# Performance work log

Measured on AMD Instinct MI355X. Metric: run time of the kernel, lower is better.

The kernel has to match this reference:

```python
import jax, jax.numpy as jnp
import numpy as np

B, C, H, W = 1, 256, 96, 96
C8 = C // 8
N = H * W


def setup_inputs() -> dict:
    key = jax.random.key(0)
    ks = jax.random.split(key, 12)
    inp = {
        "x": jax.random.normal(ks[0], (B, C, H, W), jnp.float32),
        "x_encoder": jax.random.normal(ks[1], (B, C, H, W), jnp.float32),
        # 1x1 conv params (weight stored as [out, in] matrices)
        "q_w": jax.random.normal(ks[2], (C8, C), jnp.float32) * 0.05,
        "q_b": jax.random.normal(ks[3], (C8,), jnp.float32) * 0.05,
        "k_w": jax.random.normal(ks[4], (C8, C), jnp.float32) * 0.05,
        "k_b": jax.random.normal(ks[5], (C8,), jnp.float32) * 0.05,
        "v_w": jax.random.normal(ks[6], (C, C), jnp.float32) * 0.05,
        "v_b": jax.random.normal(ks[7], (C,), jnp.float32) * 0.05,
        # positional bias parameters
        "h_pos": jax.random.normal(ks[8], (1, C8, H, 1), jnp.float32),
        "w_pos": jax.random.normal(ks[9], (1, C8, 1, W), jnp.float32),
        # gamma is zero-init in the module; use a random scalar for a non-trivial test
        "gamma": jax.random.normal(ks[10], (1,), jnp.float32),
    }
    return inp


def reference(x, x_encoder, q_w, q_b, k_w, k_b, v_w, v_b, h_pos, w_pos, gamma):
    b, c, h, w = x.shape
    n = h * w
    c8 = q_w.shape[0]
    # 1x1 convs == per-pixel linear maps
    query = (jnp.einsum('bchw,oc->bohw', x, q_w) + q_b[None, :, None, None])
    query = query.reshape(b, c8, n).transpose(0, 2, 1)            # [B, N, C8]
    key = (jnp.einsum('bchw,oc->bohw', x_encoder, k_w) + k_b[None, :, None, None])
    key = key.reshape(b, c8, n)                                   # [B, C8, N]
    # positional bias: broadcast-add then flatten, same as (height+width).view
    pos = (h_pos + w_pos).reshape(1, c8, n)                       # [1, C8, N]
    # energy = Q K^T + Q pos  ==  Q (K + pos)
    energy = jnp.einsum('bnc,bcm->bnm', query, key + pos)         # [B, N, N]
    attention = jax.nn.softmax(energy, axis=-1)
    value = (jnp.einsum('bchw,oc->bohw', x_encoder, v_w) + v_b[None, :, None, None])
    value = value.reshape(b, c, n)                                # [B, C, N]
    out = jnp.einsum('bcm,bnm->bcn', value, attention)            # [B, C, N]
    out = out.reshape(b, c, w, h)  # matches torch .view(B, C, W, H)
    return gamma * out + x
```

## Files before the change

### kernel.cpp

```cpp
#include <hip/hip_runtime.h>
#include <hip/hip_bf16.h>

#define NN 9216
#define CC 256
#define LOG2E 1.4426950408889634f

typedef __attribute__((ext_vector_type(8))) short short8;
typedef __attribute__((ext_vector_type(16))) float floatx16;
typedef __attribute__((ext_vector_type(4))) float floatx4;
typedef __attribute__((ext_vector_type(4))) unsigned short ushortx4;

#if __has_builtin(__builtin_amdgcn_exp2f)
#define fexp2 __builtin_amdgcn_exp2f
#else
#define fexp2 exp2f
#endif

__device__ __forceinline__ unsigned short f2bf(float f) {
    unsigned u = __float_as_uint(f);
    u = u + 0x7fffu + ((u >> 16) & 1u);
    return (unsigned short)(u >> 16);
}
__device__ __forceinline__ float bf2f(unsigned short s) {
    return __uint_as_float(((unsigned)s) << 16);
}
__device__ __forceinline__ unsigned pack2bf(float a, float b) {
    union { __hip_bfloat162 h; unsigned u; } cv;
    cv.h = __float22bfloat162_rn(make_float2(a, b));
    return cv.u;
}
__device__ __forceinline__ floatx16 mfma_bf16(short8 a, short8 b, floatx16 c) {
    return __builtin_amdgcn_mfma_f32_32x32x16_bf16(a, b, c, 0, 0, 0);
}

__global__ __launch_bounds__(256) void prep(
    const float* __restrict__ x, const float* __restrict__ xe,
    short* __restrict__ XBhi, short* __restrict__ XBlo,
    short* __restrict__ EBhi, short* __restrict__ EBlo)
{
    int t = threadIdx.x;
    const float* in = blockIdx.y ? xe : x;
    short* Dhi = blockIdx.y ? EBhi : XBhi;
    short* Dlo = blockIdx.y ? EBlo : XBlo;
    int tl = t & 31, sub = t >> 5;
    int nt = blockIdx.x >> 2, q4 = blockIdx.x & 3;
    int sub2 = q4 * 8 + sub;
    int kb_ = sub2 >> 1, hl = sub2 & 1;
    int n = nt * 32 + tl;
    int c0 = kb_ * 16 + hl * 8;
    union { unsigned short us[8]; short8 v8; } hi, lo;
#pragma unroll
    for (int j = 0; j < 8; ++j) {
        float val = in[(size_t)(c0 + j) * NN + n];
        unsigned short hb = f2bf(val);
        hi.us[j] = hb;
        lo.us[j] = f2bf(val - bf2f(hb));
    }
    size_t off = (((size_t)nt * 16 + kb_) * 64 + hl * 32 + tl) * 8;
    *(short8*)(Dhi + off) = hi.v8;
    *(short8*)(Dlo + off) = lo.v8;
}

__global__ __launch_bounds__(256) void wprep(
    const float* __restrict__ qw, const float* __restrict__ kw,
    const float* __restrict__ vw,
    short* __restrict__ WAhi, short* __restrict__ WAlo)
{
    int g = blockIdx.x * 256 + threadIdx.x;
    int lane = g & 63, kb_ = (g >> 6) & 15, ot = g >> 10;
    int o = lane & 31, half = lane >> 5;
    int c0 = kb_ * 16 + half * 8;
    const float* wsrc;
    int orow;
    float scale = 1.f;
    if (ot == 0) { wsrc = qw; orow = o; scale = LOG2E; }
    else if (ot == 1) { wsrc = kw; orow = o; }
    else { wsrc = vw; orow = (ot - 2) * 32 + o; }
    union { unsigned short us[8]; short8 v8; } hi, lo;
#pragma unroll
    for (int j = 0; j < 8; ++j) {
        float val = wsrc[(size_t)orow * 256 + c0 + j] * scale;
        unsigned short hb = f2bf(val);
        hi.us[j] = hb;
        lo.us[j] = f2bf(val - bf2f(hb));
    }
    size_t off = (((size_t)ot * 16 + kb_) * 64 + lane) * 8;
    *(short8*)(WAhi + off) = hi.v8;
    *(short8*)(WAlo + off) = lo.v8;
}

__global__ __launch_bounds__(256) void gemm_all(
    const short* __restrict__ XBhi, const short* __restrict__ XBlo,
    const short* __restrict__ EBhi, const short* __restrict__ EBlo,
    const short* __restrict__ WAhi, const short* __restrict__ WAlo,
    const float* __restrict__ qb, const float* __restrict__ kb,
    const float* __restrict__ hpos, const float* __restrict__ wpos,
    const float* __restrict__ vb,
    short* __restrict__ Qhi, short* __restrict__ Qlo,
    short* __restrict__ KP2, short* __restrict__ VF)
{
    __shared__ float lds[4][1024];
    int t = threadIdx.x;
    int wv = t >> 6, lane = t & 63, ln = lane & 31, h = lane >> 5;
    int nt = blockIdx.x * 2 + (wv & 1);
    int tile = blockIdx.y * 2 + (wv >> 1);

    const short* Bhi = (tile == 0 ? XBhi : EBhi) + (size_t)nt * 8192 + lane * 8;
    const short* Blo = (tile == 0 ? XBlo : EBlo) + (size_t)nt * 8192 + lane * 8;
    const short* Ahi = WAhi + (size_t)tile * 8192 + lane * 8;
    const short* Alo = WAlo + (size_t)tile * 8192 + lane * 8;

    floatx16 D;
#pragma unroll
    for (int r = 0; r < 16; ++r) D[r] = 0.f;
#pragma unroll
    for (int k = 0; k < 16; ++k) {
        short8 bh = *(const short8*)(Bhi + k * 512);
        short8 bl = *(const short8*)(Blo + k * 512);
        short8 ah = *(const short8*)(Ahi + k * 512);
        short8 al = *(const short8*)(Alo + k * 512);
        D = mfma_bf16(ah, bh, D);
        D = mfma_bf16(ah, bl, D);
        D = mfma_bf16(al, bh, D);
    }

    float* L = lds[wv];
#pragma unroll
    for (int r = 0; r < 16; ++r) {
        int row = (r & 3) + 8 * (r >> 2) + 4 * h;
        L[row * 32 + ((ln + row) & 31)] = D[r];
    }
    __syncthreads();

    if (tile == 0) {
        int n = nt * 32 + ln;
#pragma unroll
        for (int it = 0; it < 2; ++it) {
            int j0 = it * 16 + h * 8;
            union { unsigned short us[8]; short8 v8; } qh_, ql_;
#pragma unroll
            for (int jj = 0; jj < 8; ++jj) {
                int row = j0 + jj;
                float d = L[row * 32 + ((ln + row) & 31)] + qb[row] * LOG2E;
                unsigned short hb = f2bf(d);
                qh_.us[jj] = hb;
                ql_.us[jj] = f2bf(d - bf2f(hb));
            }
            *(short8*)(Qhi + (size_t)n * 32 + j0) = qh_.v8;
            *(short8*)(Qlo + (size_t)n * 32 + j0) = ql_.v8;
        }
    } else if (tile == 1) {
        int n = nt * 32 + ln;
        int hh = ((n >> 5) * 683) >> 11;
        int ww = n - hh * 96;
#pragma unroll
        for (int it = 0; it < 2; ++it) {
            int jb0 = it * 16 + h * 8;
            union { unsigned short us[8]; short8 v8; } o;
#pragma unroll
            for (int jj = 0; jj < 8; ++jj) {
                int row = jb0 + jj;
                float d = L[row * 32 + ((ln + row) & 31)]
                        + kb[row] + hpos[row * 96 + hh] + wpos[row * 96 + ww];
                o.us[jj] = f2bf(d);
            }
            *(short8*)(KP2 + (size_t)nt * 1024 + it * 512 + h * 256 + ln * 8) = o.v8;
        }
    } else {
        int cc = tile - 2;
        float bias = vb[cc * 32 + ln];
#pragma unroll
        for (int it = 0; it < 2; ++it) {
            union { unsigned short us[8]; short8 v8; } o;
#pragma unroll
            for (int ee = 0; ee < 8; ++ee) {
                int ml = it * 16 + h * 8 + ee;
                float d = L[ln * 32 + ((ml + ln) & 31)];
                o.us[ee] = f2bf(d + bias);
            }
            *(short8*)(VF + ((size_t)(nt * 2 + it) * 8 + cc) * 512 + lane * 8) = o.v8;
        }
    }
}

#define FSTEP(AH0, AH1, M0) do {                                                      \
    const size_t mo_ = (size_t)(M0) * 256;                                            \
    short8 va0 = *(const short8*)(Vb + mo_);                                          \
    short8 va1 = *(const short8*)(Vb + mo_ + 512);                                    \
    short8 va2 = *(const short8*)(Vb + mo_ + 1024);                                   \
    short8 va3 = *(const short8*)(Vb + mo_ + 1536);                                   \
    floatx16 S = {0.f,0.f,0.f,0.f,0.f,0.f,0.f,0.f,0.f,0.f,0.f,0.f,0.f,0.f,0.f,0.f};  \
    S = mfma_bf16(AH0, qf00, S);                                                      \
    S = mfma_bf16(AH0, qf01, S);                                                      \
    S = mfma_bf16(AH1, qf10, S);                                                      \
    S = mfma_bf16(AH1, qf11, S);                                                      \
    short8 va4 = *(const short8*)(Vb + mo_ + 2048);                                   \
    short8 va5 = *(const short8*)(Vb + mo_ + 2560);                                   \
    short8 va6 = *(const short8*)(Vb + mo_ + 3072);                                   \
    short8 va7 = *(const short8*)(Vb + mo_ + 3584);                                   \
    float ps = 0.f;                                                                   \
    _Pragma("unroll") for (int r = 0; r < 16; ++r) { S[r] = fexp2(S[r]); ps += S[r]; } \
    ps += __shfl_xor(ps, 32); l_run += ps;                                            \
    unsigned w0 = pack2bf(S[0], S[1]),  w1 = pack2bf(S[2], S[3]);                     \
    unsigned w2 = pack2bf(S[4], S[5]),  w3 = pack2bf(S[6], S[7]);                     \
    unsigned w4 = pack2bf(S[8], S[9]),  w5 = pack2bf(S[10], S[11]);                   \
    unsigned w6 = pack2bf(S[12], S[13]), w7 = pack2bf(S[14], S[15]);                  \
    {   unsigned p0 = h ? w0 : w2, p1 = h ? w1 : w3;                                  \
        unsigned e0 = (unsigned)__shfl_xor((int)p0, 32);                              \
        unsigned e1 = (unsigned)__shfl_xor((int)p1, 32);                              \
        union { unsigned u[4]; short8 v; } pf;                                        \
        pf.u[0] = h ? e0 : w0; pf.u[1] = h ? e1 : w1;                                 \
        pf.u[2] = h ? w2 : e0; pf.u[3] = h ? w3 : e1;                                 \
        O0 = mfma_bf16(va0, pf.v, O0); O1 = mfma_bf16(va1, pf.v, O1);                 \
        O2 = mfma_bf16(va2, pf.v, O2); O3 = mfma_bf16(va3, pf.v, O3);                 \
        O4 = mfma_bf16(va4, pf.v, O4); O5 = mfma_bf16(va5, pf.v, O5);                 \
        O6 = mfma_bf16(va6, pf.v, O6); O7 = mfma_bf16(va7, pf.v, O7); }               \
    short8 vb0 = *(const short8*)(Vb + mo_ + 4096);                                   \
    short8 vb1 = *(const short8*)(Vb + mo_ + 4608);                                   \
    short8 vb2 = *(const short8*)(Vb + mo_ + 5120);                                   \
    short8 vb3 = *(const short8*)(Vb + mo_ + 5632);                                   \
    short8 vb4 = *(const short8*)(Vb + mo_ + 6144);                                   \
    short8 vb5 = *(const short8*)(Vb + mo_ + 6656);                                   \
    short8 vb6 = *(const short8*)(Vb + mo_ + 7168);                                   \
    short8 vb7 = *(const short8*)(Vb + mo_ + 7680);                                   \
    {   unsigned p0 = h ? w4 : w6, p1 = h ? w5 : w7;                                  \
        unsigned e0 = (unsigned)__shfl_xor((int)p0, 32);                              \
        unsigned e1 = (unsigned)__shfl_xor((int)p1, 32);                              \
        union { unsigned u[4]; short8 v; } pf;                                        \
        pf.u[0] = h ? e0 : w4; pf.u[1] = h ? e1 : w5;                                 \
        pf.u[2] = h ? w6 : e0; pf.u[3] = h ? w7 : e1;                                 \
        O0 = mfma_bf16(vb0, pf.v, O0); O1 = mfma_bf16(vb1, pf.v, O1);                 \
        O2 = mfma_bf16(vb2, pf.v, O2); O3 = mfma_bf16(vb3, pf.v, O3);                 \
        O4 = mfma_bf16(vb4, pf.v, O4); O5 = mfma_bf16(vb5, pf.v, O5);                 \
        O6 = mfma_bf16(vb6, pf.v, O6); O7 = mfma_bf16(vb7, pf.v, O7); }               \
} while (0)

#define OW(G, OG) { _Pragma("unroll") for (int r = 0; r < 16; ++r) Osh[((G)*16 + r)*64 + lane] = OG[r]; }
#define OR(G, OG) { _Pragma("unroll") for (int r = 0; r < 16; ++r) OG[r] += Osh[((G)*16 + r)*64 + lane]; }
#define OGW(G, OG) { _Pragma("unroll") for (int r = 0; r < 16; ++r) { \
    int row = 32*(G) + (r & 3) + 8*(r >> 2) + 4*h;                    \
    Opart[obase + (size_t)row * NN + n0 + ln] = f2bf(OG[r]); } }

__global__ __launch_bounds__(256, 2) void flash(
    const short* __restrict__ Qhi, const short* __restrict__ Qlo,
    const short* __restrict__ KP2, const short* __restrict__ VT2,
    unsigned short* __restrict__ Opart,
    float* __restrict__ Mpart, float* __restrict__ Lpart)
{
    __shared__ float Osh[8192];
    __shared__ float Lsh[4][32];

    int t = threadIdx.x;
    int wv = t >> 6;
    int lane = t & 63;
    int ln = lane & 31;
    int h = lane >> 5;
    int nt = blockIdx.x >> 2, mq = blockIdx.x & 3;
    int n0 = nt * 32;
    int mw = mq * 2304 + wv * 576;

    int qoff = (n0 + ln) * 32 + h * 8;
    short8 qf00 = *(const short8*)(Qhi + qoff);
    short8 qf10 = *(const short8*)(Qhi + qoff + 16);
    short8 qf01 = *(const short8*)(Qlo + qoff);
    short8 qf11 = *(const short8*)(Qlo + qoff + 16);

    const short* Vb  = VT2 + (size_t)mw * 256 + (size_t)lane * 8;
    const short* KPb = KP2 + (size_t)mw * 32 + (size_t)lane * 8;

    floatx16 O0, O1, O2, O3, O4, O5, O6, O7;
#pragma unroll
    for (int r = 0; r < 16; ++r) {
        O0[r] = 0.f; O1[r] = 0.f; O2[r] = 0.f; O3[r] = 0.f;
        O4[r] = 0.f; O5[r] = 0.f; O6[r] = 0.f; O7[r] = 0.f;
    }
    float l_run = 0.f;

    short8 ahA0 = *(const short8*)(KPb);
    short8 ahA1 = *(const short8*)(KPb + 512);
    short8 ahB0, ahB1;

    for (int sp = 0; sp < 9; ++sp) {
        int m0 = sp * 64;
        ahB0 = *(const short8*)(KPb + (size_t)(m0 + 32) * 32);
        ahB1 = *(const short8*)(KPb + (size_t)(m0 + 32) * 32 + 512);
        FSTEP(ahA0, ahA1, m0);
        int nm = (sp < 8) ? (m0 + 64) : 0;
        ahA0 = *(const short8*)(KPb + (size_t)nm * 32);
        ahA1 = *(const short8*)(KPb + (size_t)nm * 32 + 512);
        FSTEP(ahB0, ahB1, m0 + 32);
    }

    if (lane < 32) Lsh[wv][ln] = l_run;
    __syncthreads();
    if (wv == 1) { OW(0,O0) OW(1,O1) OW(2,O2) OW(3,O3) OW(4,O4) OW(5,O5) OW(6,O6) OW(7,O7) }
    __syncthreads();
    if (wv == 0) { OR(0,O0) OR(1,O1) OR(2,O2) OR(3,O3) OR(4,O4) OR(5,O5) OR(6,O6) OR(7,O7) }
    __syncthreads();
    if (wv == 2) { OW(0,O0) OW(1,O1) OW(2,O2) OW(3,O3) OW(4,O4) OW(5,O5) OW(6,O6) OW(7,O7) }
    __syncthreads();
    if (wv == 0) { OR(0,O0) OR(1,O1) OR(2,O2) OR(3,O3) OR(4,O4) OR(5,O5) OR(6,O6) OR(7,O7) }
    __syncthreads();
    if (wv == 3) { OW(0,O0) OW(1,O1) OW(2,O2) OW(3,O3) OW(4,O4) OW(5,O5) OW(6,O6) OW(7,O7) }
    __syncthreads();
    if (wv == 0) {
        OR(0,O0) OR(1,O1) OR(2,O2) OR(3,O3) OR(4,O4) OR(5,O5) OR(6,O6) OR(7,O7)
        if (lane < 32) {
            Mpart[mq * NN + n0 + ln] = 0.f;
            Lpart[mq * NN + n0 + ln] = Lsh[0][ln] + Lsh[1][ln] + Lsh[2][ln] + Lsh[3][ln];
        }
        size_t obase = (size_t)mq * ((size_t)CC * NN);
        OGW(0,O0) OGW(1,O1) OGW(2,O2) OGW(3,O3) OGW(4,O4) OGW(5,O5) OGW(6,O6) OGW(7,O7)
    }
}

__global__ __launch_bounds__(256) void stats(
    const float* __restrict__ Mpart, const float* __restrict__ Lpart,
    const float* __restrict__ gamma, float* __restrict__ W)
{
    int n = blockIdx.x * 256 + threadIdx.x;
    float m[4], l[4];
#pragma unroll
    for (int q = 0; q < 4; ++q) { m[q] = Mpart[q * NN + n]; l[q] = Lpart[q * NN + n]; }
    float M = fmaxf(fmaxf(m[0], m[1]), fmaxf(m[2], m[3]));
    float e[4], L = 0.f;
#pragma unroll
    for (int q = 0; q < 4; ++q) { e[q] = fexp2(m[q] - M); L += l[q] * e[q]; }
    float g = gamma[0] / L;
#pragma unroll
    for (int q = 0; q < 4; ++q) W[q * NN + n] = e[q] * g;
}

__global__ __launch_bounds__(256) void combine(
    const unsigned short* __restrict__ Opart, const float* __restrict__ W,
    const float* __restrict__ x, float* __restrict__ out)
{
    int i = blockIdx.x * 256 + threadIdx.x;
    int flat = i * 4;
    int n = flat % NN;
    floatx4 acc = *(const floatx4*)&x[flat];
#pragma unroll
    for (int q = 0; q < 4; ++q) {
        ushortx4 o = *(const ushortx4*)(Opart + (size_t)q * ((size_t)CC * NN) + flat);
        floatx4 wq = *(const floatx4*)&W[q * NN + n];
#pragma unroll
        for (int k = 0; k < 4; ++k) acc[k] += bf2f(o[k]) * wq[k];
    }
    *(floatx4*)&out[flat] = acc;
}

extern "C" void kernel_launch(void* const* d_in, const int* in_sizes, int n_in,
                              void* d_out, int out_size, void* d_ws, size_t ws_size,
                              hipStream_t stream) {
    const float* x  = (const float*)d_in[0];
    const float* xe = (const float*)d_in[1];
    const float* qw = (const float*)d_in[2];
    const float* qb = (const float*)d_in[3];
    const float* kw = (const float*)d_in[4];
    const float* kb = (const float*)d_in[5];
    const float* vw = (const float*)d_in[6];
    const float* vb = (const float*)d_in[7];
    const float* hp = (const float*)d_in[8];
    const float* wp = (const float*)d_in[9];
    const float* gm = (const float*)d_in[10];

    char* ws = (char*)d_ws;
    short* Qhi  = (short*)(ws + 0);
    short* Qlo  = (short*)(ws + 589824);
    short* KP2  = (short*)(ws + 1179648);
    short* WAhi = (short*)(ws + 1769472);
    short* WAlo = (short*)(ws + 1933312);
    short* VF   = (short*)(ws + 2097152);
    unsigned short* Opart = (unsigned short*)(ws + 6815744);
    short* XBhi = (short*)(ws + 6815744);
    short* XBlo = (short*)(ws + 11534336);
    short* EBhi = (short*)(ws + 16252928);
    short* EBlo = (short*)(ws + 20971520);
    float* Mpart = (float*)(ws + 25690112);
    float* Lpart = (float*)(ws + 25837568);
    float* W     = (float*)(ws + 25985024);

    prep<<<dim3(1152, 2), dim3(256), 0, stream>>>(x, xe, XBhi, XBlo, EBhi, EBlo);
    wprep<<<dim3(40), dim3(256), 0, stream>>>(qw, kw, vw, WAhi, WAlo);
    gemm_all<<<dim3(144, 5), dim3(256), 0, stream>>>(
        XBhi, XBlo, EBhi, EBlo, WAhi, WAlo, qb, kb, hp, wp, vb, Qhi, Qlo, KP2, VF);
    flash<<<dim3(1152), dim3(256), 0, stream>>>(Qhi, Qlo, KP2, VF, Opart, Mpart, Lpart);
    stats<<<dim3(36), dim3(256), 0, stream>>>(Mpart, Lpart, gm, W);
    combine<<<dim3(2304), dim3(256), 0, stream>>>(Opart, W, x, (float*)d_out);
}
```

Measured before the change: 113.6 us.

## Give each flash wave its own query rows, dropping LDS cross-wave reduction

The flash kernel previously split each 32-query tile's key range across 4 waves and then summed their O accumulators through shared memory with several barriers. Now each block has 2 waves, each owning 32 queries and walking the full quarter of keys (36 steps instead of 9), so the LDS reduction, the barriers and the Mpart output go away. Because the max is fixed at zero, stats and combine are simplified to a single per-query weight applied after summing the four bf16 partials. The trade-off is fewer, smaller blocks (576 blocks of 128 threads) and longer serial loops per wave, which may reduce occupancy and latency hiding.

```diff
diff --git a/kernel.cpp b/kernel.cpp
--- a/kernel.cpp
+++ b/kernel.cpp
@@ -235,29 +235,23 @@
         O6 = mfma_bf16(vb6, pf.v, O6); O7 = mfma_bf16(vb7, pf.v, O7); }               \
 } while (0)
 
-#define OW(G, OG) { _Pragma("unroll") for (int r = 0; r < 16; ++r) Osh[((G)*16 + r)*64 + lane] = OG[r]; }
-#define OR(G, OG) { _Pragma("unroll") for (int r = 0; r < 16; ++r) OG[r] += Osh[((G)*16 + r)*64 + lane]; }
 #define OGW(G, OG) { _Pragma("unroll") for (int r = 0; r < 16; ++r) { \
     int row = 32*(G) + (r & 3) + 8*(r >> 2) + 4*h;                    \
     Opart[obase + (size_t)row * NN + n0 + ln] = f2bf(OG[r]); } }
 
-__global__ __launch_bounds__(256, 2) void flash(
+__global__ __launch_bounds__(128, 2) void flash(
     const short* __restrict__ Qhi, const short* __restrict__ Qlo,
     const short* __restrict__ KP2, const short* __restrict__ VT2,
-    unsigned short* __restrict__ Opart,
-    float* __restrict__ Mpart, float* __restrict__ Lpart)
-{
-    __shared__ float Osh[8192];
-    __shared__ float Lsh[4][32];
-
+    unsigned short* __restrict__ Opart, float* __restrict__ Lpart)
+{
     int t = threadIdx.x;
     int wv = t >> 6;
     int lane = t & 63;
     int ln = lane & 31;
     int h = lane >> 5;
     int nt = blockIdx.x >> 2, mq = blockIdx.x & 3;
-    int n0 = nt * 32;
-    int mw = mq * 2304 + wv * 576;
+    int n0 = nt * 64 + wv * 32;
+    int mstart = mq * 2304;
 
     int qoff = (n0 + ln) * 32 + h * 8;
     short8 qf00 = *(const short8*)(Qhi + qoff);
@@ -265,8 +259,8 @@
     short8 qf01 = *(const short8*)(Qlo + qoff);
     short8 qf11 = *(const short8*)(Qlo + qoff + 16);
 
-    const short* Vb  = VT2 + (size_t)mw * 256 + (size_t)lane * 8;
-    const short* KPb = KP2 + (size_t)mw * 32 + (size_t)lane * 8;
+    const short* Vb  = VT2 + (size_t)mstart * 256 + (size_t)lane * 8;
+    const short* KPb = KP2 + (size_t)mstart * 32 + (size_t)lane * 8;
 
     floatx16 O0, O1, O2, O3, O4, O5, O6, O7;
 #pragma unroll
@@ -280,55 +274,29 @@
     short8 ahA1 = *(const short8*)(KPb + 512);
     short8 ahB0, ahB1;
 
-    for (int sp = 0; sp < 9; ++sp) {
+    for (int sp = 0; sp < 36; ++sp) {
         int m0 = sp * 64;
         ahB0 = *(const short8*)(KPb + (size_t)(m0 + 32) * 32);
         ahB1 = *(const short8*)(KPb + (size_t)(m0 + 32) * 32 + 512);
         FSTEP(ahA0, ahA1, m0);
-        int nm = (sp < 8) ? (m0 + 64) : 0;
+        int nm = (sp < 35) ? (m0 + 64) : 0;
         ahA0 = *(const short8*)(KPb + (size_t)nm * 32);
         ahA1 = *(const short8*)(KPb + (size_t)nm * 32 + 512);
         FSTEP(ahB0, ahB1, m0 + 32);
     }
 
-    if (lane < 32) Lsh[wv][ln] = l_run;
-    __syncthreads();
-    if (wv == 1) { OW(0,O0) OW(1,O1) OW(2,O2) OW(3,O3) OW(4,O4) OW(5,O5) OW(6,O6) OW(7,O7) }
-    __syncthreads();
-    if (wv == 0) { OR(0,O0) OR(1,O1) OR(2,O2) OR(3,O3) OR(4,O4) OR(5,O5) OR(6,O6) OR(7,O7) }
-    __syncthreads();
-    if (wv == 2) { OW(0,O0) OW(1,O1) OW(2,O2) OW(3,O3) OW(4,O4) OW(5,O5) OW(6,O6) OW(7,O7) }
-    __syncthreads();
-    if (wv == 0) { OR(0,O0) OR(1,O1) OR(2,O2) OR(3,O3) OR(4,O4) OR(5,O5) OR(6,O6) OR(7,O7) }
-    __syncthreads();
-    if (wv == 3) { OW(0,O0) OW(1,O1) OW(2,O2) OW(3,O3) OW(4,O4) OW(5,O5) OW(6,O6) OW(7,O7) }
-    __syncthreads();
-    if (wv == 0) {
-        OR(0,O0) OR(1,O1) OR(2,O2) OR(3,O3) OR(4,O4) OR(5,O5) OR(6,O6) OR(7,O7)
-        if (lane < 32) {
-            Mpart[mq * NN + n0 + ln] = 0.f;
-            Lpart[mq * NN + n0 + ln] = Lsh[0][ln] + Lsh[1][ln] + Lsh[2][ln] + Lsh[3][ln];
-        }
-        size_t obase = (size_t)mq * ((size_t)CC * NN);
-        OGW(0,O0) OGW(1,O1) OGW(2,O2) OGW(3,O3) OGW(4,O4) OGW(5,O5) OGW(6,O6) OGW(7,O7)
-    }
+    if (lane < 32) Lpart[mq * NN + n0 + ln] = l_run;
+    size_t obase = (size_t)mq * ((size_t)CC * NN);
+    OGW(0,O0) OGW(1,O1) OGW(2,O2) OGW(3,O3) OGW(4,O4) OGW(5,O5) OGW(6,O6) OGW(7,O7)
 }
 
 __global__ __launch_bounds__(256) void stats(
-    const float* __restrict__ Mpart, const float* __restrict__ Lpart,
-    const float* __restrict__ gamma, float* __restrict__ W)
+    const float* __restrict__ Lpart, const float* __restrict__ gamma,
+    float* __restrict__ W)
 {
     int n = blockIdx.x * 256 + threadIdx.x;
-    float m[4], l[4];
-#pragma unroll
-    for (int q = 0; q < 4; ++q) { m[q] = Mpart[q * NN + n]; l[q] = Lpart[q * NN + n]; }
-    float M = fmaxf(fmaxf(m[0], m[1]), fmaxf(m[2], m[3]));
-    float e[4], L = 0.f;
-#pragma unroll
-    for (int q = 0; q < 4; ++q) { e[q] = fexp2(m[q] - M); L += l[q] * e[q]; }
-    float g = gamma[0] / L;
-#pragma unroll
-    for (int q = 0; q < 4; ++q) W[q * NN + n] = e[q] * g;
+    float L = Lpart[n] + Lpart[NN + n] + Lpart[2 * NN + n] + Lpart[3 * NN + n];
+    W[n] = gamma[0] / L;
 }
 
 __global__ __launch_bounds__(256) void combine(
@@ -339,13 +307,14 @@
     int flat = i * 4;
     int n = flat % NN;
     floatx4 acc = *(const floatx4*)&x[flat];
+    floatx4 w = *(const floatx4*)&W[n];
+    float s0 = 0.f, s1 = 0.f, s2 = 0.f, s3 = 0.f;
 #pragma unroll
     for (int q = 0; q < 4; ++q) {
         ushortx4 o = *(const ushortx4*)(Opart + (size_t)q * ((size_t)CC * NN) + flat);
-        floatx4 wq = *(const floatx4*)&W[q * NN + n];
-#pragma unroll
-        for (int k = 0; k < 4; ++k) acc[k] += bf2f(o[k]) * wq[k];
-    }
+        s0 += bf2f(o[0]); s1 += bf2f(o[1]); s2 += bf2f(o[2]); s3 += bf2f(o[3]);
+    }
+    acc[0] += s0 * w[0]; acc[1] += s1 * w[1]; acc[2] += s2 * w[2]; acc[3] += s3 * w[3];
     *(floatx4*)&out[flat] = acc;
 }
 
@@ -376,7 +345,6 @@
     short* XBlo = (short*)(ws + 11534336);
     short* EBhi = (short*)(ws + 16252928);
     short* EBlo = (short*)(ws + 20971520);
-    float* Mpart = (float*)(ws + 25690112);
     float* Lpart = (float*)(ws + 25837568);
     float* W     = (float*)(ws + 25985024);
 
@@ -384,7 +352,7 @@
     wprep<<<dim3(40), dim3(256), 0, stream>>>(qw, kw, vw, WAhi, WAlo);
     gemm_all<<<dim3(144, 5), dim3(256), 0, stream>>>(
         XBhi, XBlo, EBhi, EBlo, WAhi, WAlo, qb, kb, hp, wp, vb, Qhi, Qlo, KP2, VF);
-    flash<<<dim3(1152), dim3(256), 0, stream>>>(Qhi, Qlo, KP2, VF, Opart, Mpart, Lpart);
-    stats<<<dim3(36), dim3(256), 0, stream>>>(Mpart, Lpart, gm, W);
+    flash<<<dim3(576), dim3(128), 0, stream>>>(Qhi, Qlo, KP2, VF, Opart, Lpart);
+    stats<<<dim3(36), dim3(256), 0, stream>>>(Lpart, gm, W);
     combine<<<dim3(2304), dim3(256), 0, stream>>>(Opart, W, x, (float*)d_out);
 }
```

Measured after the change: 112.2 us. Within noise of the previous version (-1.2%).
